# Optimization experiments

Measured on AMD Instinct MI355X. Metric: run time of the kernel, lower is better.

Reference implementation:

```python
import jax, jax.numpy as jnp
import numpy as np

B, T, K = 1024, 512, 64
START, STOP = K - 2, K - 1
NEG = -10000.0


def setup_inputs() -> dict:
    key = jax.random.key(0)
    k1, k2, k3, k4 = jax.random.split(key, 4)
    feats = jax.random.normal(k1, (B, T, K), dtype=jnp.float32)
    lengths = jax.random.randint(k2, (B,), 1, T + 1)  # valid seq lengths in [1, T]
    tags = jax.random.randint(k3, (B, T), 0, K)
    transitions = jax.random.normal(k4, (K, K), dtype=jnp.float32)
    # CRF constraints: nothing transitions INTO start, nothing transitions OUT of stop
    transitions = transitions.at[START, :].set(NEG).at[:, STOP].set(NEG)
    return {"feats": feats, "lengths": lengths, "tags": tags, "transitions": transitions}


def _forward_alg(feats, transitions, lengths):
    Bn, Tn, Kn = feats.shape
    alpha0 = jnp.full((Bn, Kn), NEG, feats.dtype).at[:, START].set(0.0)

    def step(alpha, emit):  # alpha: [B,K] over prev tag j; emit: [B,K] over cur tag i
        # tag_var[b,i,j] = emit[b,i] + trans[i,j] + alpha[b,j]
        new = jax.nn.logsumexp(emit[:, :, None] + transitions[None, :, :] + alpha[:, None, :], axis=2)
        return new, new

    _, ys = jax.lax.scan(step, alpha0, jnp.swapaxes(feats, 0, 1))  # ys: [T,B,K]
    all_alpha = jnp.concatenate([alpha0[None], ys], axis=0)  # [T+1,B,K]
    sel = all_alpha[lengths, jnp.arange(Bn)]  # alpha after `lengths` steps: [B,K]
    terminal = sel + transitions[STOP][None, :]
    return jax.nn.logsumexp(terminal, axis=1)  # [B]


def _score_sentence(feats, transitions, lengths, tags):
    Bn, Tn, Kn = feats.shape
    pad_start = jnp.concatenate([jnp.full((Bn, 1), START, tags.dtype), tags], axis=1)  # [B,T+1]
    pad_stop = jnp.concatenate([tags, jnp.full((Bn, 1), STOP, tags.dtype)], axis=1)  # [B,T+1]
    pos = jnp.arange(Tn + 1)[None, :]
    pad_stop = jnp.where(pos >= lengths[:, None], STOP, pad_stop)  # tags[lengths:] -> STOP
    trans_vals = transitions[pad_stop, pad_start]  # [B,T+1]
    trans_score = jnp.sum(jnp.where(pos <= lengths[:, None], trans_vals, 0.0), axis=1)
    emit_vals = jnp.take_along_axis(feats, tags[:, :, None], axis=2)[:, :, 0]  # [B,T]
    emit_mask = jnp.arange(Tn)[None, :] < lengths[:, None]
    emit_score = jnp.sum(jnp.where(emit_mask, emit_vals, 0.0), axis=1)
    return trans_score + emit_score


def reference(feats, lengths, tags, transitions):
    forward_score = _forward_alg(feats, transitions, lengths)
    gold_score = _score_sentence(feats, transitions, lengths, tags)
    return jnp.mean(forward_score - gold_score)
```

## Files before the change

kernel.cpp:

```cpp
#include <hip/hip_runtime.h>

#define CRF_B 1024
#define CRF_T 512
#define CRF_K 64
#define CRF_START 62
#define CRF_STOP 63

__device__ __forceinline__ float bcastf(float v, int lane) {
  return __int_as_float(__builtin_amdgcn_readlane(__float_as_int(v), lane));
}

__device__ __forceinline__ float wave_max64(float v) {
#pragma unroll
  for (int off = 32; off > 0; off >>= 1) v = fmaxf(v, __shfl_xor(v, off, 64));
  return v;
}

__device__ __forceinline__ float wave_sum64(float v) {
#pragma unroll
  for (int off = 32; off > 0; off >>= 1) v += __shfl_xor(v, off, 64);
  return v;
}

__global__ __launch_bounds__(64, 1) void crf_fwd_kernel(
    const float* __restrict__ feats, const int* __restrict__ lengths,
    const int* __restrict__ tags, const float* __restrict__ trans,
    float* __restrict__ out) {
  __shared__ float sT[CRF_K * 65];
  __shared__ int sTags[CRF_T];

  const int b = blockIdx.x;
  const int lane = threadIdx.x;

  for (int k = 0; k < CRF_K; ++k) sT[k * 65 + lane] = trans[k * CRF_K + lane];

  const int* btags = tags + b * CRF_T;
#pragma unroll
  for (int t = lane; t < CRF_T; t += 64) sTags[t] = btags[t];

  __syncthreads();

  float E[CRF_K];
#pragma unroll
  for (int j = 0; j < CRF_K; ++j) E[j] = __expf(sT[lane * 65 + j]);

  const int L = lengths[b];
  const float* bfeats = feats + (size_t)b * CRF_T * CRF_K;

  float alpha = (lane == CRF_START) ? 0.0f : -10000.0f;
  float goldE = 0.0f;
  float goldT = 0.0f;
  int prev = CRF_START;

  float e0 = bfeats[0 * CRF_K + lane];
  float e1 = bfeats[1 * CRF_K + lane];
  float e2 = bfeats[2 * CRF_K + lane];
  float e3 = bfeats[3 * CRF_K + lane];

  auto do_step = [&](float m, float emit_t, int t) {
    float p = __expf(alpha - m);
    float a0 = 0.f, a1 = 0.f, a2 = 0.f, a3 = 0.f;
#pragma unroll
    for (int j = 0; j < CRF_K; j += 4) {
      a0 = __builtin_fmaf(E[j + 0], bcastf(p, j + 0), a0);
      a1 = __builtin_fmaf(E[j + 1], bcastf(p, j + 1), a1);
      a2 = __builtin_fmaf(E[j + 2], bcastf(p, j + 2), a2);
      a3 = __builtin_fmaf(E[j + 3], bcastf(p, j + 3), a3);
    }
    float s = (a0 + a1) + (a2 + a3);
    alpha = emit_t + m + __logf(s);
    int tg = sTags[t];
    goldE += __shfl(emit_t, tg, 64);
    goldT += sT[tg * 65 + prev];
    prev = tg;
  };

  const int Lb = L & ~3;
  for (int t0 = 0; t0 < Lb; t0 += 4) {
    const int tn = t0 + 4;
    float f0 = 0.f, f1 = 0.f, f2 = 0.f, f3 = 0.f;
    if (tn < CRF_T) {
      const float* pb = bfeats + tn * CRF_K + lane;
      f0 = pb[0];
      f1 = pb[CRF_K];
      f2 = pb[2 * CRF_K];
      f3 = pb[3 * CRF_K];
    }
    float m = wave_max64(alpha);
    do_step(m, e0, t0);
    do_step(m, e1, t0 + 1);
    do_step(m, e2, t0 + 2);
    do_step(m, e3, t0 + 3);
    e0 = f0; e1 = f1; e2 = f2; e3 = f3;
  }
  for (int t = Lb; t < L; ++t) {
    float m = wave_max64(alpha);
    float em = (t - Lb == 0) ? e0 : ((t - Lb == 1) ? e1 : e2);
    do_step(m, em, t);
  }

  goldT += sT[CRF_STOP * 65 + prev];

  float v = alpha + sT[CRF_STOP * 65 + lane];
  float m2 = wave_max64(v);
  float s2 = wave_sum64(__expf(v - m2));
  float fwd = m2 + __logf(s2);

  if (lane == 0) {
    atomicAdd(out, (fwd - (goldE + goldT)) * (1.0f / CRF_B));
  }
}

extern "C" void kernel_launch(void* const* d_in, const int* in_sizes, int n_in,
                              void* d_out, int out_size, void* d_ws, size_t ws_size,
                              hipStream_t stream) {
  const float* feats = (const float*)d_in[0];
  const int* lengths = (const int*)d_in[1];
  const int* tags = (const int*)d_in[2];
  const float* trans = (const float*)d_in[3];
  float* out = (float*)d_out;
  hipMemsetAsync(out, 0, sizeof(float), stream);
  crf_fwd_kernel<<<CRF_B, 64, 0, stream>>>(feats, lengths, tags, trans, out);
}
```

Baseline: 348.0 us.

## Run forward recursion in scaled probability space and split gold score onto second wave

The forward recursion now keeps probabilities instead of log-alphas, so each step needs only one multiply by exp(emit) rather than a log. Renormalization by the wave max, with an accumulated log offset, happens once every 8 steps, and the unroll grows from 4 to 8. The gold-path score moves to a second wavefront in the same block, which computes it in parallel over time steps instead of serially inside the recursion. Going 8 steps without rescaling risks overflow or underflow when transition and emission magnitudes are large.

```diff
diff --git a/kernel.cpp b/kernel.cpp
--- a/kernel.cpp
+++ b/kernel.cpp
@@ -22,92 +22,114 @@
   return v;
 }
 
-__global__ __launch_bounds__(64, 1) void crf_fwd_kernel(
+__global__ __launch_bounds__(128, 1) void crf_kernel(
     const float* __restrict__ feats, const int* __restrict__ lengths,
     const int* __restrict__ tags, const float* __restrict__ trans,
     float* __restrict__ out) {
   __shared__ float sT[CRF_K * 65];
-  __shared__ int sTags[CRF_T];
 
   const int b = blockIdx.x;
-  const int lane = threadIdx.x;
+  const int tid = threadIdx.x;
+  const int lane = tid & 63;
 
-  for (int k = 0; k < CRF_K; ++k) sT[k * 65 + lane] = trans[k * CRF_K + lane];
-
-  const int* btags = tags + b * CRF_T;
-#pragma unroll
-  for (int t = lane; t < CRF_T; t += 64) sTags[t] = btags[t];
-
+  for (int idx = tid; idx < CRF_K * CRF_K; idx += 128)
+    sT[(idx >> 6) * 65 + (idx & 63)] = trans[idx];
   __syncthreads();
 
-  float E[CRF_K];
+  const int L = lengths[b];
+
+  if (tid < 64) {
+    float E[CRF_K];
 #pragma unroll
-  for (int j = 0; j < CRF_K; ++j) E[j] = __expf(sT[lane * 65 + j]);
+    for (int j = 0; j < CRF_K; ++j) E[j] = __expf(sT[lane * 65 + j]);
 
-  const int L = lengths[b];
-  const float* bfeats = feats + (size_t)b * CRF_T * CRF_K;
+    const float* bfeats = feats + (size_t)b * CRF_T * CRF_K + lane;
 
-  float alpha = (lane == CRF_START) ? 0.0f : -10000.0f;
-  float goldE = 0.0f;
-  float goldT = 0.0f;
-  int prev = CRF_START;
+    float P = (lane == CRF_START) ? 1.0f : 0.0f;
+    float offset = 0.0f;
 
-  float e0 = bfeats[0 * CRF_K + lane];
-  float e1 = bfeats[1 * CRF_K + lane];
-  float e2 = bfeats[2 * CRF_K + lane];
-  float e3 = bfeats[3 * CRF_K + lane];
+    float e[8], f[8];
+#pragma unroll
+    for (int r = 0; r < 8; ++r) e[r] = bfeats[r * CRF_K];
 
-  auto do_step = [&](float m, float emit_t, int t) {
-    float p = __expf(alpha - m);
-    float a0 = 0.f, a1 = 0.f, a2 = 0.f, a3 = 0.f;
+    const int Lb = L & ~7;
+    for (int t0 = 0; t0 < Lb; t0 += 8) {
+      const int tn = t0 + 8;
+      if (tn < CRF_T) {
 #pragma unroll
-    for (int j = 0; j < CRF_K; j += 4) {
-      a0 = __builtin_fmaf(E[j + 0], bcastf(p, j + 0), a0);
-      a1 = __builtin_fmaf(E[j + 1], bcastf(p, j + 1), a1);
-      a2 = __builtin_fmaf(E[j + 2], bcastf(p, j + 2), a2);
-      a3 = __builtin_fmaf(E[j + 3], bcastf(p, j + 3), a3);
+        for (int r = 0; r < 8; ++r) f[r] = bfeats[(tn + r) * CRF_K];
+      } else {
+#pragma unroll
+        for (int r = 0; r < 8; ++r) f[r] = 0.0f;
+      }
+      float ee[8];
+#pragma unroll
+      for (int r = 0; r < 8; ++r) ee[r] = __expf(e[r]);
+
+      float M = wave_max64(P);
+      offset += __logf(M);
+      P *= __builtin_amdgcn_rcpf(M);
+
+#pragma unroll
+      for (int r = 0; r < 8; ++r) {
+        float a0 = 0.f, a1 = 0.f, a2 = 0.f, a3 = 0.f;
+#pragma unroll
+        for (int j = 0; j < CRF_K; j += 4) {
+          a0 = __builtin_fmaf(E[j + 0], bcastf(P, j + 0), a0);
+          a1 = __builtin_fmaf(E[j + 1], bcastf(P, j + 1), a1);
+          a2 = __builtin_fmaf(E[j + 2], bcastf(P, j + 2), a2);
+          a3 = __builtin_fmaf(E[j + 3], bcastf(P, j + 3), a3);
+        }
+        P = ((a0 + a1) + (a2 + a3)) * ee[r];
+      }
+#pragma unroll
+      for (int r = 0; r < 8; ++r) e[r] = f[r];
     }
-    float s = (a0 + a1) + (a2 + a3);
-    alpha = emit_t + m + __logf(s);
-    int tg = sTags[t];
-    goldE += __shfl(emit_t, tg, 64);
-    goldT += sT[tg * 65 + prev];
-    prev = tg;
-  };
 
-  const int Lb = L & ~3;
-  for (int t0 = 0; t0 < Lb; t0 += 4) {
-    const int tn = t0 + 4;
-    float f0 = 0.f, f1 = 0.f, f2 = 0.f, f3 = 0.f;
-    if (tn < CRF_T) {
-      const float* pb = bfeats + tn * CRF_K + lane;
-      f0 = pb[0];
-      f1 = pb[CRF_K];
-      f2 = pb[2 * CRF_K];
-      f3 = pb[3 * CRF_K];
+    if (Lb < L) {
+      float M = wave_max64(P);
+      offset += __logf(M);
+      P *= __builtin_amdgcn_rcpf(M);
+#pragma unroll
+      for (int r = 0; r < 8; ++r) {
+        if (Lb + r < L) {
+          float ee = __expf(e[r]);
+          float a0 = 0.f, a1 = 0.f, a2 = 0.f, a3 = 0.f;
+#pragma unroll
+          for (int j = 0; j < CRF_K; j += 4) {
+            a0 = __builtin_fmaf(E[j + 0], bcastf(P, j + 0), a0);
+            a1 = __builtin_fmaf(E[j + 1], bcastf(P, j + 1), a1);
+            a2 = __builtin_fmaf(E[j + 2], bcastf(P, j + 2), a2);
+            a3 = __builtin_fmaf(E[j + 3], bcastf(P, j + 3), a3);
+          }
+          P = ((a0 + a1) + (a2 + a3)) * ee;
+        }
+      }
     }
-    float m = wave_max64(alpha);
-    do_step(m, e0, t0);
-    do_step(m, e1, t0 + 1);
-    do_step(m, e2, t0 + 2);
-    do_step(m, e3, t0 + 3);
-    e0 = f0; e1 = f1; e2 = f2; e3 = f3;
-  }
-  for (int t = Lb; t < L; ++t) {
-    float m = wave_max64(alpha);
-    float em = (t - Lb == 0) ? e0 : ((t - Lb == 1) ? e1 : e2);
-    do_step(m, em, t);
-  }
 
-  goldT += sT[CRF_STOP * 65 + prev];
-
-  float v = alpha + sT[CRF_STOP * 65 + lane];
-  float m2 = wave_max64(v);
-  float s2 = wave_sum64(__expf(v - m2));
-  float fwd = m2 + __logf(s2);
-
-  if (lane == 0) {
-    atomicAdd(out, (fwd - (goldE + goldT)) * (1.0f / CRF_B));
+    float eST = __expf(sT[CRF_STOP * 65 + lane]);
+    float s2 = wave_sum64(P * eST);
+    float fwd = offset + __logf(s2);
+    if (lane == 0) atomicAdd(out, fwd * (1.0f / CRF_B));
+  } else {
+    const int* btags = tags + b * CRF_T;
+    const float* bf = feats + (size_t)b * CRF_T * CRF_K;
+    float gold = 0.0f;
+#pragma unroll
+    for (int base = 0; base < CRF_T; base += 64) {
+      int t = base + lane;
+      if (t < L) {
+        int tg = btags[t];
+        int tp = (t == 0) ? CRF_START : btags[t - 1];
+        gold += bf[(size_t)t * CRF_K + tg];
+        gold += sT[tg * 65 + tp];
+      }
+    }
+    gold = wave_sum64(gold);
+    if (lane == 0) {
+      gold += sT[CRF_STOP * 65 + btags[L - 1]];
+      atomicAdd(out, -gold * (1.0f / CRF_B));
+    }
   }
 }
 
@@ -120,5 +142,5 @@
   const float* trans = (const float*)d_in[3];
   float* out = (float*)d_out;
   hipMemsetAsync(out, 0, sizeof(float), stream);
-  crf_fwd_kernel<<<CRF_B, 64, 0, stream>>>(feats, lengths, tags, trans, out);
+  crf_kernel<<<CRF_B, 128, 0, stream>>>(feats, lengths, tags, trans, out);
 }
```

New measurement: 309.5 us. 11.1% less time.
